# Kernel optimization log

Measured on AMD Instinct MI355X. Metric: run time of the kernel, lower is better.

## Reference

```python
import jax, jax.numpy as jnp
import numpy as np

N_NODES = 100000
N_EDGES = 1200000
N_GRAPHS = 8
IN_DIM = 64
HID = 64
N_CLASSES = 2


def setup_inputs() -> dict:
    key = jax.random.key(0)
    ks = jax.random.split(key, 8)
    features = jax.random.normal(ks[0], (N_NODES, IN_DIM), dtype=jnp.float32)
    W1 = jax.random.normal(ks[1], (IN_DIM, HID), dtype=jnp.float32) * (1.0 / np.sqrt(IN_DIM))
    b1 = jnp.zeros((HID,), dtype=jnp.float32)
    W2 = jax.random.normal(ks[2], (HID, HID), dtype=jnp.float32) * (1.0 / np.sqrt(HID))
    b2 = jnp.zeros((HID,), dtype=jnp.float32)
    Wp = jax.random.normal(ks[3], (HID, N_CLASSES), dtype=jnp.float32) * (1.0 / np.sqrt(HID))
    bp = jnp.zeros((N_CLASSES,), dtype=jnp.float32)
    edge_src = jax.random.randint(ks[4], (N_EDGES,), 0, N_NODES, dtype=jnp.int64 if jax.config.jax_enable_x64 else jnp.int32)
    edge_dst = jax.random.randint(ks[5], (N_EDGES,), 0, N_NODES, dtype=edge_src.dtype)
    graph_id = jnp.sort(jax.random.randint(ks[6], (N_NODES,), 0, N_GRAPHS, dtype=edge_src.dtype))
    return {"features": features, "W1": W1, "b1": b1, "W2": W2, "b2": b2,
            "Wp": Wp, "bp": bp, "edge_src": edge_src, "edge_dst": edge_dst,
            "graph_id": graph_id}


def reference(features, W1, b1, W2, b2, Wp, bp, edge_src, edge_dst, graph_id):
    N = features.shape[0]
    dt = features.dtype
    ones_e = jnp.ones(edge_src.shape[0], dtype=dt)
    # DGL GraphConv norm='both': symmetric normalization with out-deg (src) / in-deg (dst)
    out_deg = jnp.clip(jax.ops.segment_sum(ones_e, edge_src, num_segments=N), 1.0)
    in_deg = jnp.clip(jax.ops.segment_sum(ones_e, edge_dst, num_segments=N), 1.0)
    src_norm = jax.lax.rsqrt(out_deg)[:, None]  # [N,1]
    dst_norm = jax.lax.rsqrt(in_deg)[:, None]   # [N,1]

    def gconv(h, W, b):
        h = h * src_norm
        msgs = h[edge_src]                                    # [E, d] gather
        agg = jax.ops.segment_sum(msgs, edge_dst, num_segments=N)  # [N, d]
        agg = agg * dst_norm
        return jax.nn.relu(agg @ W + b)

    h = gconv(features, W1, b1)   # [N, HID]
    h = gconv(h, W2, b2)          # [N, HID]

    # dgl.mean_nodes: per-graph mean pooling
    cnt = jnp.clip(jax.ops.segment_sum(jnp.ones(N, dtype=dt), graph_id, num_segments=N_GRAPHS), 1.0)
    hg = jax.ops.segment_sum(h, graph_id, num_segments=N_GRAPHS) / cnt[:, None]  # [G, HID]
    return hg @ Wp + bp
```

## Files before the change

### kernel.cpp

```cpp
#include <hip/hip_runtime.h>

#define NN 100000
#define NE 1200000
#define NG 8
#define DIM 64
#define WROW 64
#define SCAN_BS 256
#define NB ((NN + SCAN_BS - 1) / SCAN_BS)
#define COLCAP (NE + 7 * NN)

#define RANGE 16384
#define RSH 14
#define NR 7
#define GSL 28
#define SLICE4 ((NE / 4 + GSL - 1) / GSL)

__global__ __launch_bounds__(256) void hist_kernel(const int4* __restrict__ esrc4,
                                                   const int4* __restrict__ edst4,
                                                   int* __restrict__ partial) {
  __shared__ int h[RANGE];
  int job = blockIdx.x;
  int g = job % GSL;
  int r = (job / GSL) % NR;
  int dir = job / (GSL * NR);
  const int4* __restrict__ idx = dir ? edst4 : esrc4;
  int lo = r * RANGE, hi = min(lo + RANGE, NN);
  for (int i = threadIdx.x; i < RANGE / 4; i += 256) ((int4*)h)[i] = make_int4(0, 0, 0, 0);
  __syncthreads();
  int s0 = g * SLICE4, s1 = min(s0 + SLICE4, NE / 4);
  for (int i = s0 + threadIdx.x; i < s1; i += 256) {
    int4 v = idx[i];
    if (v.x >= lo && v.x < hi) atomicAdd(&h[v.x - lo], 1);
    if (v.y >= lo && v.y < hi) atomicAdd(&h[v.y - lo], 1);
    if (v.z >= lo && v.z < hi) atomicAdd(&h[v.z - lo], 1);
    if (v.w >= lo && v.w < hi) atomicAdd(&h[v.w - lo], 1);
  }
  __syncthreads();
  int4* dst = (int4*)(partial + (size_t)job * RANGE);
  int cap4 = (hi - lo) >> 2;
  for (int i = threadIdx.x; i < cap4; i += 256) dst[i] = ((int4*)h)[i];
}

__global__ __launch_bounds__(SCAN_BS) void scan1_kernel(const int* __restrict__ partial,
                                                        float* __restrict__ snormA,
                                                        float* __restrict__ dnormA,
                                                        int* __restrict__ rp2,
                                                        int* __restrict__ bsum, int N) {
  __shared__ int t[SCAN_BS];
  int i = blockIdx.x * SCAN_BS + threadIdx.x;
  int v = 0;
  if (i < N) {
    int r = i >> RSH, off = i & (RANGE - 1);
    const int* ps = partial + ((size_t)r * GSL) * RANGE + off;
    const int* pd = partial + (((size_t)NR + r) * GSL) * RANGE + off;
    int sOut = 0, sIn = 0;
#pragma unroll
    for (int g = 0; g < GSL; ++g) {
      sOut += ps[(size_t)g * RANGE];
      sIn += pd[(size_t)g * RANGE];
    }
    snormA[i] = rsqrtf(fmaxf((float)sOut, 1.0f));
    dnormA[i] = rsqrtf(fmaxf((float)sIn, 1.0f));
    v = (sIn + 7) & ~7;
  }
  t[threadIdx.x] = v;
  __syncthreads();
  for (int off = 1; off < SCAN_BS; off <<= 1) {
    int u = (threadIdx.x >= off) ? t[threadIdx.x - off] : 0;
    __syncthreads();
    t[threadIdx.x] += u;
    __syncthreads();
  }
  if (i < N) rp2[i] = t[threadIdx.x] - v;
  if (i == N - 1) rp2[N] = t[threadIdx.x];
  if (threadIdx.x == SCAN_BS - 1) bsum[blockIdx.x] = t[threadIdx.x];
}

__global__ __launch_bounds__(512) void scan2_kernel(const int* __restrict__ bsum,
                                                    int* __restrict__ boff, int nb) {
  __shared__ int t[512];
  int v = ((int)threadIdx.x < nb) ? bsum[threadIdx.x] : 0;
  t[threadIdx.x] = v;
  __syncthreads();
  for (int off = 1; off < 512; off <<= 1) {
    int u = (threadIdx.x >= off) ? t[threadIdx.x - off] : 0;
    __syncthreads();
    t[threadIdx.x] += u;
    __syncthreads();
  }
  boff[threadIdx.x] = t[threadIdx.x] - v;
}

__global__ __launch_bounds__(SCAN_BS) void scan3_kernel(int* __restrict__ rp2,
                                                        const int* __restrict__ boff, int N) {
  int i = blockIdx.x * SCAN_BS + threadIdx.x;
  if (i < N) rp2[i] += boff[blockIdx.x];
  if (i == N - 1) rp2[N] += boff[blockIdx.x];
}

__global__ void offscan_kernel(int* __restrict__ partial, const int* __restrict__ rp2, int N) {
  int n = blockIdx.x * blockDim.x + threadIdx.x;
  if (n >= N) return;
  int r = n >> RSH, i = n & (RANGE - 1);
  int* p = partial + (((size_t)NR + r) * GSL) * RANGE + i;
  int running = rp2[n];
#pragma unroll
  for (int g = 0; g < GSL; ++g) {
    int tmp = p[(size_t)g * RANGE];
    p[(size_t)g * RANGE] = running;
    running += tmp;
  }
}

__global__ void colinit_kernel(int4* __restrict__ col4, int n4) {
  int i = blockIdx.x * blockDim.x + threadIdx.x;
  int st = gridDim.x * blockDim.x;
  for (; i < n4; i += st) col4[i] = make_int4(NN, NN, NN, NN);
}

__global__ __launch_bounds__(256) void fill_kernel(const int4* __restrict__ esrc4,
                                                   const int4* __restrict__ edst4,
                                                   const int* __restrict__ partial,
                                                   int* __restrict__ col) {
  __shared__ int cnt[RANGE];
  int job = blockIdx.x;
  int g = job % GSL, r = job / GSL;
  int lo = r * RANGE, hi = min(lo + RANGE, NN);
  const int* off = partial + (((size_t)NR + r) * GSL + g) * RANGE;
  for (int i = threadIdx.x; i < hi - lo; i += 256) cnt[i] = off[i];
  __syncthreads();
  int s0 = g * SLICE4, s1 = min(s0 + SLICE4, NE / 4);
  for (int i = s0 + threadIdx.x; i < s1; i += 256) {
    int4 d = edst4[i];
    int4 s = esrc4[i];
    if (d.x >= lo && d.x < hi) col[atomicAdd(&cnt[d.x - lo], 1)] = s.x;
    if (d.y >= lo && d.y < hi) col[atomicAdd(&cnt[d.y - lo], 1)] = s.y;
    if (d.z >= lo && d.z < hi) col[atomicAdd(&cnt[d.z - lo], 1)] = s.z;
    if (d.w >= lo && d.w < hi) col[atomicAdd(&cnt[d.w - lo], 1)] = s.w;
  }
}

template <int PRESCALED, int POOL>
__global__ __launch_bounds__(256) void gconv_kernel(
    const float* __restrict__ xs, const float* __restrict__ snormA, const float* __restrict__ dnormA,
    const int* __restrict__ rp2, const int* __restrict__ col,
    const float* __restrict__ W, const float* __restrict__ b,
    float* __restrict__ out, const int* __restrict__ gid,
    float* __restrict__ gsum, float* __restrict__ gcnt, int N) {
  __shared__ float Wt[DIM * WROW];
  __shared__ float aL[4][4][DIM];
  __shared__ float lsum[NG * DIM];
  __shared__ float lcnt[NG];
  for (int i = threadIdx.x; i < DIM * 16; i += 256) {
    int k = i >> 4, ch = i & 15;
    *(float4*)&Wt[k * WROW + ch * 4] = *(const float4*)(W + k * DIM + ch * 4);
  }
  if (POOL) {
    for (int i = threadIdx.x; i < NG * DIM; i += 256) lsum[i] = 0.0f;
    if (threadIdx.x < NG) lcnt[threadIdx.x] = 0.0f;
  }
  __syncthreads();

  const int lane = threadIdx.x & 63;
  const int wid = threadIdx.x >> 6;
  const int g = lane >> 4;
  const int idx = lane & 15;
  const int t4 = idx << 2;
  const float4 bb = *(const float4*)(b + t4);
  const int waveId = blockIdx.x * 4 + wid;
  const int stride4 = gridDim.x * 16;

  for (int n4 = waveId * 4; n4 < N; n4 += stride4) {
    int n = n4 + g;
    bool valid = n < N;
    int nc = valid ? n : 0;
    int base = rp2[nc];
    int end = rp2[nc + 1];
    float4 acc = make_float4(0.f, 0.f, 0.f, 0.f);
    float4 acc2 = make_float4(0.f, 0.f, 0.f, 0.f);
    for (int p = base; p < end; p += 8) {
      int4 c0 = *(const int4*)(col + p);
      int4 c1 = *(const int4*)(col + p + 4);
      if (PRESCALED) {
        float4 v0 = *(const float4*)(xs + (size_t)c0.x * DIM + t4);
        float4 v1 = *(const float4*)(xs + (size_t)c0.y * DIM + t4);
        float4 v2 = *(const float4*)(xs + (size_t)c0.z * DIM + t4);
        float4 v3 = *(const float4*)(xs + (size_t)c0.w * DIM + t4);
        float4 v4 = *(const float4*)(xs + (size_t)c1.x * DIM + t4);
        float4 v5 = *(const float4*)(xs + (size_t)c1.y * DIM + t4);
        float4 v6 = *(const float4*)(xs + (size_t)c1.z * DIM + t4);
        float4 v7 = *(const float4*)(xs + (size_t)c1.w * DIM + t4);
        acc.x += (v0.x + v1.x) + (v2.x + v3.x);
        acc.y += (v0.y + v1.y) + (v2.y + v3.y);
        acc.z += (v0.z + v1.z) + (v2.z + v3.z);
        acc.w += (v0.w + v1.w) + (v2.w + v3.w);
        acc2.x += (v4.x + v5.x) + (v6.x + v7.x);
        acc2.y += (v4.y + v5.y) + (v6.y + v7.y);
        acc2.z += (v4.z + v5.z) + (v6.z + v7.z);
        acc2.w += (v4.w + v5.w) + (v6.w + v7.w);
      } else {
        float w0 = snormA[c0.x], w1 = snormA[c0.y], w2 = snormA[c0.z], w3 = snormA[c0.w];
        float w4 = snormA[c1.x], w5 = snormA[c1.y], w6 = snormA[c1.z], w7 = snormA[c1.w];
        int s0 = min(c0.x, NN - 1), s1 = min(c0.y, NN - 1);
        int s2 = min(c0.z, NN - 1), s3 = min(c0.w, NN - 1);
        int s4 = min(c1.x, NN - 1), s5 = min(c1.y, NN - 1);
        int s6 = min(c1.z, NN - 1), s7 = min(c1.w, NN - 1);
        float4 v0 = *(const float4*)(xs + (size_t)s0 * DIM + t4);
        float4 v1 = *(const float4*)(xs + (size_t)s1 * DIM + t4);
        float4 v2 = *(const float4*)(xs + (size_t)s2 * DIM + t4);
        float4 v3 = *(const float4*)(xs + (size_t)s3 * DIM + t4);
        float4 v4 = *(const float4*)(xs + (size_t)s4 * DIM + t4);
        float4 v5 = *(const float4*)(xs + (size_t)s5 * DIM + t4);
        float4 v6 = *(const float4*)(xs + (size_t)s6 * DIM + t4);
        float4 v7 = *(const float4*)(xs + (size_t)s7 * DIM + t4);
        acc.x = fmaf(v0.x, w0, fmaf(v1.x, w1, fmaf(v2.x, w2, fmaf(v3.x, w3, acc.x))));
        acc.y = fmaf(v0.y, w0, fmaf(v1.y, w1, fmaf(v2.y, w2, fmaf(v3.y, w3, acc.y))));
        acc.z = fmaf(v0.z, w0, fmaf(v1.z, w1, fmaf(v2.z, w2, fmaf(v3.z, w3, acc.z))));
        acc.w = fmaf(v0.w, w0, fmaf(v1.w, w1, fmaf(v2.w, w2, fmaf(v3.w, w3, acc.w))));
        acc2.x = fmaf(v4.x, w4, fmaf(v5.x, w5, fmaf(v6.x, w6, fmaf(v7.x, w7, acc2.x))));
        acc2.y = fmaf(v4.y, w4, fmaf(v5.y, w5, fmaf(v6.y, w6, fmaf(v7.y, w7, acc2.y))));
        acc2.z = fmaf(v4.z, w4, fmaf(v5.z, w5, fmaf(v6.z, w6, fmaf(v7.z, w7, acc2.z))));
        acc2.w = fmaf(v4.w, w4, fmaf(v5.w, w5, fmaf(v6.w, w6, fmaf(v7.w, w7, acc2.w))));
      }
    }
    float dn = dnormA[nc];
    acc.x = (acc.x + acc2.x) * dn;
    acc.y = (acc.y + acc2.y) * dn;
    acc.z = (acc.z + acc2.z) * dn;
    acc.w = (acc.w + acc2.w) * dn;

    *(float4*)&aL[wid][g][t4] = acc;

    float4 r = bb;
#pragma unroll
    for (int kc = 0; kc < 16; ++kc) {
      float4 av = *(const float4*)&aL[wid][g][4 * kc];
      float4 w0 = *(const float4*)(Wt + (4 * kc + 0) * WROW + t4);
      float4 w1 = *(const float4*)(Wt + (4 * kc + 1) * WROW + t4);
      float4 w2 = *(const float4*)(Wt + (4 * kc + 2) * WROW + t4);
      float4 w3 = *(const float4*)(Wt + (4 * kc + 3) * WROW + t4);
      r.x = fmaf(av.x, w0.x, r.x); r.y = fmaf(av.x, w0.y, r.y);
      r.z = fmaf(av.x, w0.z, r.z); r.w = fmaf(av.x, w0.w, r.w);
      r.x = fmaf(av.y, w1.x, r.x); r.y = fmaf(av.y, w1.y, r.y);
      r.z = fmaf(av.y, w1.z, r.z); r.w = fmaf(av.y, w1.w, r.w);
      r.x = fmaf(av.z, w2.x, r.x); r.y = fmaf(av.z, w2.y, r.y);
      r.z = fmaf(av.z, w2.z, r.z); r.w = fmaf(av.z, w2.w, r.w);
      r.x = fmaf(av.w, w3.x, r.x); r.y = fmaf(av.w, w3.y, r.y);
      r.z = fmaf(av.w, w3.z, r.z); r.w = fmaf(av.w, w3.w, r.w);
    }
    r.x = fmaxf(r.x, 0.f); r.y = fmaxf(r.y, 0.f);
    r.z = fmaxf(r.z, 0.f); r.w = fmaxf(r.w, 0.f);

    if (POOL) {
      if (valid) {
        int gi = gid[n];
        atomicAdd(&lsum[gi * DIM + t4 + 0], r.x);
        atomicAdd(&lsum[gi * DIM + t4 + 1], r.y);
        atomicAdd(&lsum[gi * DIM + t4 + 2], r.z);
        atomicAdd(&lsum[gi * DIM + t4 + 3], r.w);
        if (idx == 0) atomicAdd(&lcnt[gi], 1.0f);
      }
    } else if (valid) {
      float sn = snormA[n];
      float4 o = make_float4(r.x * sn, r.y * sn, r.z * sn, r.w * sn);
      *(float4*)(out + (size_t)n * DIM + t4) = o;
    }
  }

  if (POOL) {
    __syncthreads();
    for (int i = threadIdx.x; i < NG * DIM; i += 256) atomicAdd(&gsum[i], lsum[i]);
    if (threadIdx.x < NG) atomicAdd(&gcnt[threadIdx.x], lcnt[threadIdx.x]);
  }
}

__global__ void final_kernel(const float* __restrict__ gsum, const float* __restrict__ gcnt,
                             const float* __restrict__ Wp, const float* __restrict__ bp,
                             float* __restrict__ out) {
  int lane = threadIdx.x;
#pragma unroll
  for (int g = 0; g < NG; ++g) {
    float inv = 1.0f / fmaxf(gcnt[g], 1.0f);
    float hv = gsum[g * DIM + lane] * inv;
#pragma unroll
    for (int c = 0; c < 2; ++c) {
      float p = hv * Wp[lane * 2 + c];
      for (int off = 32; off; off >>= 1) p += __shfl_down(p, off, 64);
      if (lane == 0) out[g * 2 + c] = p + bp[c];
    }
  }
}

extern "C" void kernel_launch(void* const* d_in, const int* in_sizes, int n_in,
                              void* d_out, int out_size, void* d_ws, size_t ws_size,
                              hipStream_t stream) {
  const float* features = (const float*)d_in[0];
  const float* W1 = (const float*)d_in[1];
  const float* b1 = (const float*)d_in[2];
  const float* W2 = (const float*)d_in[3];
  const float* b2 = (const float*)d_in[4];
  const float* Wp = (const float*)d_in[5];
  const float* bp = (const float*)d_in[6];
  const int* esrc = (const int*)d_in[7];
  const int* edst = (const int*)d_in[8];
  const int* gid = (const int*)d_in[9];
  float* out = (float*)d_out;

  const int N = NN;
  const size_t NPART = (size_t)2 * NR * GSL * RANGE;

  float* base = (float*)d_ws;
  size_t off = 0;
  auto alloc = [&](size_t nwords) { size_t r = off; off = (off + nwords + 15) & ~(size_t)15; return r; };

  float* gsum = base + alloc(NG * DIM);
  float* gcnt = base + alloc(NG);
  size_t zeroWords = off;
  float* snormA = base + alloc(N + 1);
  float* dnormA = base + alloc(N);
  int* rp2   = (int*)(base + alloc(N + 1));
  int* bsum  = (int*)(base + alloc(512));
  int* boff  = (int*)(base + alloc(512));
  int* col   = (int*)(base + alloc(COLCAP));
  int* partial = (int*)(base + alloc(NPART));
  float* B   = base + alloc((size_t)(N + 1) * DIM);

  hipMemsetAsync(d_ws, 0, zeroWords * sizeof(float), stream);
  hipMemsetAsync(snormA + N, 0, sizeof(float), stream);
  hipMemsetAsync(B + (size_t)N * DIM, 0, DIM * sizeof(float), stream);

  hist_kernel<<<2 * NR * GSL, 256, 0, stream>>>((const int4*)esrc, (const int4*)edst, partial);

  scan1_kernel<<<NB, SCAN_BS, 0, stream>>>(partial, snormA, dnormA, rp2, bsum, N);
  scan2_kernel<<<1, 512, 0, stream>>>(bsum, boff, NB);
  scan3_kernel<<<NB, SCAN_BS, 0, stream>>>(rp2, boff, N);

  offscan_kernel<<<(NR * RANGE + 255) / 256, 256, 0, stream>>>(partial, rp2, N);
  colinit_kernel<<<(COLCAP / 4 + 255) / 256, 256, 0, stream>>>((int4*)col, COLCAP / 4);
  fill_kernel<<<NR * GSL, 256, 0, stream>>>((const int4*)esrc, (const int4*)edst, partial, col);

  gconv_kernel<0, 0><<<2048, 256, 0, stream>>>(features, snormA, dnormA, rp2, col, W1, b1,
                                               B, gid, gsum, gcnt, N);
  gconv_kernel<1, 1><<<2048, 256, 0, stream>>>(B, snormA, dnormA, rp2, col, W2, b2,
                                               nullptr, gid, gsum, gcnt, N);

  final_kernel<<<1, 64, 0, stream>>>(gsum, gcnt, Wp, bp, out);
}
```

Measured before the change: 247.9 us.

## Store prescaled node features in bf16 to halve gather traffic

Adds a prescale kernel that multiplies the input features by the source norm and packs them to bf16. Both gconv layers now gather bf16 rows, and layer one writes its output in bf16. This removes the per-edge snorm lookups in the first layer and halves the bytes fetched by the random gathers, at the cost of an extra pass over the features and reduced precision in the aggregated messages.

```diff
diff --git a/kernel.cpp b/kernel.cpp
--- a/kernel.cpp
+++ b/kernel.cpp
@@ -14,6 +14,13 @@
 #define NR 7
 #define GSL 28
 #define SLICE4 ((NE / 4 + GSL - 1) / GSL)
+
+__device__ __forceinline__ unsigned bf16rne(float f) {
+  unsigned u = __float_as_uint(f);
+  return (u + 0x7FFF + ((u >> 16) & 1)) >> 16;
+}
+__device__ __forceinline__ float bflo(unsigned u) { return __uint_as_float(u << 16); }
+__device__ __forceinline__ float bfhi(unsigned u) { return __uint_as_float(u & 0xFFFF0000u); }
 
 __global__ __launch_bounds__(256) void hist_kernel(const int4* __restrict__ esrc4,
                                                    const int4* __restrict__ edst4,
@@ -140,12 +147,30 @@
   }
 }
 
-template <int PRESCALED, int POOL>
+__global__ void prescale_kernel(const float* __restrict__ f, const float* __restrict__ snormA,
+                                unsigned short* __restrict__ xb, int N) {
+  int i = blockIdx.x * blockDim.x + threadIdx.x;
+  if (i < N * 8) {
+    int n = i >> 3;
+    float sn = snormA[n];
+    const float4* p = (const float4*)(f + (size_t)i * 8);
+    float4 a = p[0], b = p[1];
+    uint4 o;
+    o.x = bf16rne(a.x * sn) | (bf16rne(a.y * sn) << 16);
+    o.y = bf16rne(a.z * sn) | (bf16rne(a.w * sn) << 16);
+    o.z = bf16rne(b.x * sn) | (bf16rne(b.y * sn) << 16);
+    o.w = bf16rne(b.z * sn) | (bf16rne(b.w * sn) << 16);
+    ((uint4*)xb)[i] = o;
+  }
+}
+
+template <int POOL>
 __global__ __launch_bounds__(256) void gconv_kernel(
-    const float* __restrict__ xs, const float* __restrict__ snormA, const float* __restrict__ dnormA,
+    const unsigned short* __restrict__ xb, const float* __restrict__ snormA,
+    const float* __restrict__ dnormA,
     const int* __restrict__ rp2, const int* __restrict__ col,
     const float* __restrict__ W, const float* __restrict__ b,
-    float* __restrict__ out, const int* __restrict__ gid,
+    unsigned short* __restrict__ outb, const int* __restrict__ gid,
     float* __restrict__ gsum, float* __restrict__ gcnt, int N) {
   __shared__ float Wt[DIM * WROW];
   __shared__ float aL[4][4][DIM];
@@ -181,47 +206,22 @@
     for (int p = base; p < end; p += 8) {
       int4 c0 = *(const int4*)(col + p);
       int4 c1 = *(const int4*)(col + p + 4);
-      if (PRESCALED) {
-        float4 v0 = *(const float4*)(xs + (size_t)c0.x * DIM + t4);
-        float4 v1 = *(const float4*)(xs + (size_t)c0.y * DIM + t4);
-        float4 v2 = *(const float4*)(xs + (size_t)c0.z * DIM + t4);
-        float4 v3 = *(const float4*)(xs + (size_t)c0.w * DIM + t4);
-        float4 v4 = *(const float4*)(xs + (size_t)c1.x * DIM + t4);
-        float4 v5 = *(const float4*)(xs + (size_t)c1.y * DIM + t4);
-        float4 v6 = *(const float4*)(xs + (size_t)c1.z * DIM + t4);
-        float4 v7 = *(const float4*)(xs + (size_t)c1.w * DIM + t4);
-        acc.x += (v0.x + v1.x) + (v2.x + v3.x);
-        acc.y += (v0.y + v1.y) + (v2.y + v3.y);
-        acc.z += (v0.z + v1.z) + (v2.z + v3.z);
-        acc.w += (v0.w + v1.w) + (v2.w + v3.w);
-        acc2.x += (v4.x + v5.x) + (v6.x + v7.x);
-        acc2.y += (v4.y + v5.y) + (v6.y + v7.y);
-        acc2.z += (v4.z + v5.z) + (v6.z + v7.z);
-        acc2.w += (v4.w + v5.w) + (v6.w + v7.w);
-      } else {
-        float w0 = snormA[c0.x], w1 = snormA[c0.y], w2 = snormA[c0.z], w3 = snormA[c0.w];
-        float w4 = snormA[c1.x], w5 = snormA[c1.y], w6 = snormA[c1.z], w7 = snormA[c1.w];
-        int s0 = min(c0.x, NN - 1), s1 = min(c0.y, NN - 1);
-        int s2 = min(c0.z, NN - 1), s3 = min(c0.w, NN - 1);
-        int s4 = min(c1.x, NN - 1), s5 = min(c1.y, NN - 1);
-        int s6 = min(c1.z, NN - 1), s7 = min(c1.w, NN - 1);
-        float4 v0 = *(const float4*)(xs + (size_t)s0 * DIM + t4);
-        float4 v1 = *(const float4*)(xs + (size_t)s1 * DIM + t4);
-        float4 v2 = *(const float4*)(xs + (size_t)s2 * DIM + t4);
-        float4 v3 = *(const float4*)(xs + (size_t)s3 * DIM + t4);
-        float4 v4 = *(const float4*)(xs + (size_t)s4 * DIM + t4);
-        float4 v5 = *(const float4*)(xs + (size_t)s5 * DIM + t4);
-        float4 v6 = *(const float4*)(xs + (size_t)s6 * DIM + t4);
-        float4 v7 = *(const float4*)(xs + (size_t)s7 * DIM + t4);
-        acc.x = fmaf(v0.x, w0, fmaf(v1.x, w1, fmaf(v2.x, w2, fmaf(v3.x, w3, acc.x))));
-        acc.y = fmaf(v0.y, w0, fmaf(v1.y, w1, fmaf(v2.y, w2, fmaf(v3.y, w3, acc.y))));
-        acc.z = fmaf(v0.z, w0, fmaf(v1.z, w1, fmaf(v2.z, w2, fmaf(v3.z, w3, acc.z))));
-        acc.w = fmaf(v0.w, w0, fmaf(v1.w, w1, fmaf(v2.w, w2, fmaf(v3.w, w3, acc.w))));
-        acc2.x = fmaf(v4.x, w4, fmaf(v5.x, w5, fmaf(v6.x, w6, fmaf(v7.x, w7, acc2.x))));
-        acc2.y = fmaf(v4.y, w4, fmaf(v5.y, w5, fmaf(v6.y, w6, fmaf(v7.y, w7, acc2.y))));
-        acc2.z = fmaf(v4.z, w4, fmaf(v5.z, w5, fmaf(v6.z, w6, fmaf(v7.z, w7, acc2.z))));
-        acc2.w = fmaf(v4.w, w4, fmaf(v5.w, w5, fmaf(v6.w, w6, fmaf(v7.w, w7, acc2.w))));
-      }
+      uint2 u0 = *(const uint2*)(xb + ((size_t)c0.x << 6) + t4);
+      uint2 u1 = *(const uint2*)(xb + ((size_t)c0.y << 6) + t4);
+      uint2 u2 = *(const uint2*)(xb + ((size_t)c0.z << 6) + t4);
+      uint2 u3 = *(const uint2*)(xb + ((size_t)c0.w << 6) + t4);
+      uint2 u4 = *(const uint2*)(xb + ((size_t)c1.x << 6) + t4);
+      uint2 u5 = *(const uint2*)(xb + ((size_t)c1.y << 6) + t4);
+      uint2 u6 = *(const uint2*)(xb + ((size_t)c1.z << 6) + t4);
+      uint2 u7 = *(const uint2*)(xb + ((size_t)c1.w << 6) + t4);
+      acc.x += (bflo(u0.x) + bflo(u1.x)) + (bflo(u2.x) + bflo(u3.x));
+      acc.y += (bfhi(u0.x) + bfhi(u1.x)) + (bfhi(u2.x) + bfhi(u3.x));
+      acc.z += (bflo(u0.y) + bflo(u1.y)) + (bflo(u2.y) + bflo(u3.y));
+      acc.w += (bfhi(u0.y) + bfhi(u1.y)) + (bfhi(u2.y) + bfhi(u3.y));
+      acc2.x += (bflo(u4.x) + bflo(u5.x)) + (bflo(u6.x) + bflo(u7.x));
+      acc2.y += (bfhi(u4.x) + bfhi(u5.x)) + (bfhi(u6.x) + bfhi(u7.x));
+      acc2.z += (bflo(u4.y) + bflo(u5.y)) + (bflo(u6.y) + bflo(u7.y));
+      acc2.w += (bfhi(u4.y) + bfhi(u5.y)) + (bfhi(u6.y) + bfhi(u7.y));
     }
     float dn = dnormA[nc];
     acc.x = (acc.x + acc2.x) * dn;
@@ -262,8 +262,10 @@
       }
     } else if (valid) {
       float sn = snormA[n];
-      float4 o = make_float4(r.x * sn, r.y * sn, r.z * sn, r.w * sn);
-      *(float4*)(out + (size_t)n * DIM + t4) = o;
+      uint2 o;
+      o.x = bf16rne(r.x * sn) | (bf16rne(r.y * sn) << 16);
+      o.y = bf16rne(r.z * sn) | (bf16rne(r.w * sn) << 16);
+      *(uint2*)(outb + ((size_t)n << 6) + t4) = o;
     }
   }
 
@@ -316,18 +318,19 @@
   float* gsum = base + alloc(NG * DIM);
   float* gcnt = base + alloc(NG);
   size_t zeroWords = off;
-  float* snormA = base + alloc(N + 1);
+  float* snormA = base + alloc(N);
   float* dnormA = base + alloc(N);
   int* rp2   = (int*)(base + alloc(N + 1));
   int* bsum  = (int*)(base + alloc(512));
   int* boff  = (int*)(base + alloc(512));
   int* col   = (int*)(base + alloc(COLCAP));
   int* partial = (int*)(base + alloc(NPART));
-  float* B   = base + alloc((size_t)(N + 1) * DIM);
+  unsigned short* xb = (unsigned short*)(base + alloc((size_t)(N + 1) * DIM / 2));
+  unsigned short* Bb = (unsigned short*)(base + alloc((size_t)(N + 1) * DIM / 2));
 
   hipMemsetAsync(d_ws, 0, zeroWords * sizeof(float), stream);
-  hipMemsetAsync(snormA + N, 0, sizeof(float), stream);
-  hipMemsetAsync(B + (size_t)N * DIM, 0, DIM * sizeof(float), stream);
+  hipMemsetAsync(xb + (size_t)N * DIM, 0, DIM * sizeof(unsigned short), stream);
+  hipMemsetAsync(Bb + (size_t)N * DIM, 0, DIM * sizeof(unsigned short), stream);
 
   hist_kernel<<<2 * NR * GSL, 256, 0, stream>>>((const int4*)esrc, (const int4*)edst, partial);
 
@@ -339,10 +342,12 @@
   colinit_kernel<<<(COLCAP / 4 + 255) / 256, 256, 0, stream>>>((int4*)col, COLCAP / 4);
   fill_kernel<<<NR * GSL, 256, 0, stream>>>((const int4*)esrc, (const int4*)edst, partial, col);
 
-  gconv_kernel<0, 0><<<2048, 256, 0, stream>>>(features, snormA, dnormA, rp2, col, W1, b1,
-                                               B, gid, gsum, gcnt, N);
-  gconv_kernel<1, 1><<<2048, 256, 0, stream>>>(B, snormA, dnormA, rp2, col, W2, b2,
-                                               nullptr, gid, gsum, gcnt, N);
+  prescale_kernel<<<(N * 8 + 255) / 256, 256, 0, stream>>>(features, snormA, xb, N);
+
+  gconv_kernel<0><<<2048, 256, 0, stream>>>(xb, snormA, dnormA, rp2, col, W1, b1,
+                                            Bb, gid, gsum, gcnt, N);
+  gconv_kernel<1><<<2048, 256, 0, stream>>>(Bb, snormA, dnormA, rp2, col, W2, b2,
+                                            nullptr, gid, gsum, gcnt, N);
 
   final_kernel<<<1, 64, 0, stream>>>(gsum, gcnt, Wp, bp, out);
 }
```

New measurement: 226.6 us. -8.6%, faster.
